# Optimization experiments

Measured on AMD Instinct MI355X. Metric: run time of the kernel, lower is better.

## Reference

```python
import jax, jax.numpy as jnp
import numpy as np

N_NODES = 100000


def setup_inputs() -> dict:
    key = jax.random.key(0)
    k1, k2, k3, k4, k5 = jax.random.split(key, 5)
    E = 3200000
    F_IN, F_OUT = 128, 128
    x = jax.random.normal(k1, (N_NODES, F_IN), dtype=jnp.float32)
    row = jax.random.randint(k2, (E,), 0, N_NODES, dtype=jnp.int32)
    col = jax.random.randint(k3, (E,), 0, N_NODES, dtype=jnp.int32)
    # normalized-adjacency-like positive values
    edge_vals = jax.random.uniform(k4, (E,), dtype=jnp.float32)
    # xavier_uniform for W, zeros for bias (reset_parameters)
    limit = float(np.sqrt(6.0 / (F_IN + F_OUT)))
    W = jax.random.uniform(k5, (F_IN, F_OUT), dtype=jnp.float32, minval=-limit, maxval=limit)
    b = jnp.zeros((F_OUT,), dtype=jnp.float32)
    return {"x": x, "row": row, "col": col, "edge_vals": edge_vals, "W": W, "b": b}


def reference(x, row, col, edge_vals, W, b):
    # SpMM: (A @ x) where A is COO (row, col, edge_vals) of shape [N, N]
    gathered = edge_vals[:, None] * x[col]            # [E, F_in] irregular gather
    ax = jax.ops.segment_sum(gathered, row, num_segments=N_NODES)  # [N, F_in]
    # dense GEMM + bias
    return ax @ W + b
```

## Files before the change

### kernel.cpp

```cpp
#include <hip/hip_runtime.h>


#define FDIM 128
#define RPB   64
#define NBMAX 2048
#define MAXB  2560
#define TILE  4096

typedef __attribute__((ext_vector_type(8))) short short8;
typedef __attribute__((ext_vector_type(4))) float f32x4;

__device__ __forceinline__ unsigned bf16rn(float f) {
    unsigned u = __float_as_uint(f);
    return (u + 0x7FFFu + ((u >> 16) & 1u)) >> 16;
}

__global__ __launch_bounds__(256) void prep_w(const float* __restrict__ W,
                                              ushort* __restrict__ wbf) {
    int i = blockIdx.x * 1024 + threadIdx.x;
#pragma unroll
    for (int t = 0; t < 4; ++t, i += 256) {
        int k = i >> 7, c = i & 127;
        wbf[(c * 256 + ((k * 2) ^ ((c & 7) << 4))) >> 1] = (ushort)bf16rn(W[i]);
    }
}

__global__ __launch_bounds__(256) void fat_gemm_binA(
        const float* __restrict__ x, const ushort* __restrict__ wbf,
        char* __restrict__ xwq, float* __restrict__ sglob,
        const int* __restrict__ row, const int* __restrict__ col,
        const float* __restrict__ ev,
        int* __restrict__ bucketcur, unsigned long long* __restrict__ bentry,
        int N, int E, int nb, int G1, int G2) {
    __shared__ char smem[32768];
    const int tid = threadIdx.x;
    const int bid = blockIdx.x;

    if (bid < G1) {
        {
            const uint4* wsrc = (const uint4*)wbf;
            uint4* wdst = (uint4*)smem;
#pragma unroll
            for (int i = 0; i < 8; ++i) wdst[i * 256 + tid] = wsrc[i * 256 + tid];
        }
        __syncthreads();

        const int w = tid >> 6, l = tid & 63;
        const int g = l >> 4, c = l & 15;
        const int rbase = bid * 64 + w * 16;
        const int arow = rbase + c;
        const int kgrp = g * 8;

        f32x4 acc[8];
#pragma unroll
        for (int nt = 0; nt < 8; ++nt) acc[nt] = (f32x4){0.f, 0.f, 0.f, 0.f};

#pragma unroll
        for (int kb = 0; kb < 4; ++kb) {
            short8 a;
            if (arow < N) {
                const float* xp = x + (size_t)arow * FDIM + kb * 32 + kgrp;
                float4 x0 = ((const float4*)xp)[0];
                float4 x1 = ((const float4*)xp)[1];
                a[0] = (short)bf16rn(x0.x); a[1] = (short)bf16rn(x0.y);
                a[2] = (short)bf16rn(x0.z); a[3] = (short)bf16rn(x0.w);
                a[4] = (short)bf16rn(x1.x); a[5] = (short)bf16rn(x1.y);
                a[6] = (short)bf16rn(x1.z); a[7] = (short)bf16rn(x1.w);
            } else {
#pragma unroll
                for (int j = 0; j < 8; ++j) a[j] = 0;
            }
            const int kbyte = kb * 64 + g * 16;
#pragma unroll
            for (int nt = 0; nt < 8; ++nt) {
                int cc = nt * 16 + c;
                short8 bfrag = *(const short8*)(smem + cc * 256 + (kbyte ^ ((cc & 7) << 4)));
                acc[nt] = __builtin_amdgcn_mfma_f32_16x16x32_bf16(a, bfrag, acc[nt], 0, 0, 0);
            }
        }

        __syncthreads();

        float sr[4], inv[4];
#pragma unroll
        for (int r = 0; r < 4; ++r) {
            float m = 0.f;
#pragma unroll
            for (int nt = 0; nt < 8; ++nt) m = fmaxf(m, fabsf(acc[nt][r]));
#pragma unroll
            for (int mk = 1; mk < 16; mk <<= 1) m = fmaxf(m, __shfl_xor(m, mk));
            sr[r]  = m * (1.0f / 127.0f);
            inv[r] = (m > 0.f) ? (127.0f / m) : 0.f;
        }
        if (c == 0) {
#pragma unroll
            for (int r = 0; r < 4; ++r) {
                int gr = rbase + g * 4 + r;
                if (gr < N) sglob[gr] = sr[r];
            }
        }
        char* qlds = smem + w * 2048;
#pragma unroll
        for (int r = 0; r < 4; ++r)
#pragma unroll
            for (int nt = 0; nt < 8; ++nt) {
                int qi = (int)rintf(acc[nt][r] * inv[r]);
                qlds[(g * 4 + r) * 128 + nt * 16 + c] = (char)qi;
            }
        __syncthreads();

        uint4* dst = (uint4*)(xwq + (size_t)bid * 8192);
        const uint4* srcq = (const uint4*)smem;
#pragma unroll
        for (int t = 0; t < 2; ++t) {
            int i = t * 256 + tid;
            if (bid * 64 + (i >> 3) < N) dst[i] = srcq[i];
        }
    } else {
        int* tcnt  = (int*)smem;
        int* tbase = (int*)(smem + NBMAX * 4);

        for (long long t0 = (long long)(bid - G1) * TILE; t0 < E;
             t0 += (long long)G2 * TILE) {
            for (int i = tid; i < nb; i += 256) tcnt[i] = 0;
            __syncthreads();

            unsigned long long pk[16];
            int rr[16];
#pragma unroll
            for (int j = 0; j < 16; ++j) {
                long long e = t0 + j * 256 + tid;
                if (e < E) {
                    int r = row[e];
                    int cc = col[e];
                    unsigned evu = __float_as_uint(ev[e]);
                    pk[j] = ((unsigned long long)(unsigned)r << 47) |
                            ((unsigned long long)(unsigned)cc << 30) |
                            (unsigned long long)(evu >> 2);
                    rr[j] = r;
                    atomicAdd(&tcnt[r >> 6], 1);
                } else {
                    rr[j] = -1;
                }
            }
            __syncthreads();

            for (int i = tid; i < nb; i += 256) {
                int cc = tcnt[i];
                tbase[i] = cc ? atomicAdd(&bucketcur[i], cc) : 0;
                tcnt[i] = 0;
            }
            __syncthreads();

#pragma unroll
            for (int j = 0; j < 16; ++j) {
                if (rr[j] >= 0) {
                    int bk = rr[j] >> 6;
                    int pos = tbase[bk] + atomicAdd(&tcnt[bk], 1);
                    if (pos < MAXB) bentry[(size_t)bk * MAXB + pos] = pk[j];
                }
            }
            __syncthreads();
        }
    }
}

#define PBATCH(B)                                                                \
    {                                                                            \
        int2 p[B];                                                               \
        _Pragma("unroll") for (int j = 0; j < B; ++j) p[j] = sent[e + 2*j + h];  \
        unsigned xv[B];                                                          \
        _Pragma("unroll") for (int j = 0; j < B; ++j)                            \
            xv[j] = *(const unsigned*)(xwq + (unsigned)p[j].x + loff);           \
        _Pragma("unroll") for (int j = 0; j < B; ++j) {                          \
            float v = __int_as_float(p[j].y);                                    \
            float fx = (float)(signed char)(xv[j] & 0xFF);                       \
            float fy = (float)(signed char)((xv[j] >> 8) & 0xFF);                \
            float fz = (float)(signed char)((xv[j] >> 16) & 0xFF);               \
            float fw = (float)(signed char)(xv[j] >> 24);                        \
            if (j & 1) {                                                         \
                a1.x = fmaf(v, fx, a1.x); a1.y = fmaf(v, fy, a1.y);              \
                a1.z = fmaf(v, fz, a1.z); a1.w = fmaf(v, fw, a1.w);              \
            } else {                                                             \
                a0.x = fmaf(v, fx, a0.x); a0.y = fmaf(v, fy, a0.y);              \
                a0.z = fmaf(v, fz, a0.z); a0.w = fmaf(v, fw, a0.w);              \
            }                                                                    \
        }                                                                        \
    }

__global__ __launch_bounds__(256) void sort_gather(
        const char* __restrict__ xwq, const float* __restrict__ sglob,
        const unsigned long long* __restrict__ bentry,
        const int* __restrict__ bucketcur,
        const float* __restrict__ bias, float* __restrict__ out, int N) {
    __shared__ int2 sent[MAXB];
    __shared__ int cnt[RPB];
    __shared__ int rs[RPB + 1];
    __shared__ int cur[RPB];
    const int tid = threadIdx.x;
    const int b = blockIdx.x;

    int sz = bucketcur[b];
    if (sz > MAXB) sz = MAXB;
    const unsigned long long* src = bentry + (size_t)b * MAXB;

    if (tid < RPB) cnt[tid] = 0;
    __syncthreads();

    unsigned long long pk[10];
    float sc[10];
#pragma unroll
    for (int k = 0; k < 10; ++k) {
        int i = tid + k * 256;
        if (i < sz) {
            unsigned long long p = src[i];
            pk[k] = p;
            atomicAdd(&cnt[(int)(p >> 47) & (RPB - 1)], 1);
            sc[k] = sglob[(unsigned)(p >> 30) & 0x1FFFFu];
        }
    }
    __syncthreads();

    if (tid < 64) {
        int v = cnt[tid];
        int s = v;
#pragma unroll
        for (int off = 1; off < 64; off <<= 1) {
            int t = __shfl_up(s, off);
            if (tid >= off) s += t;
        }
        rs[tid] = s - v;
        cur[tid] = s - v;
        if (tid == 63) rs[64] = s;
    }
    __syncthreads();

#pragma unroll
    for (int k = 0; k < 10; ++k) {
        int i = tid + k * 256;
        if (i < sz) {
            unsigned long long p = pk[k];
            int rib = (int)(p >> 47) & (RPB - 1);
            unsigned coff = (((unsigned)(p >> 30)) & 0x1FFFFu) << 7;
            float evf = __uint_as_float(((unsigned)p & 0x3FFFFFFFu) << 2);
            int pos = atomicAdd(&cur[rib], 1);
            sent[pos] = make_int2((int)coff, __float_as_int(evf * sc[k]));
        }
    }
    __syncthreads();

    const int lane = tid & 63;
    const int wid  = tid >> 6;
    const int h    = lane >> 5;
    const int s    = lane & 31;
    const unsigned loff = (unsigned)(s << 2);
    float4 bias4 = ((const float4*)bias)[s];
    const float4 zero4 = {0.f, 0.f, 0.f, 0.f};

    for (int rl = 0; rl < 16; ++rl) {
        const int rib = wid * 16 + rl;
        const int gr = b * RPB + rib;
        int e = rs[rib];
        const int end = rs[rib + 1];

        float4 a0 = (h == 0) ? bias4 : zero4;
        float4 a1 = zero4;

        for (; e + 8 <= end; e += 8) PBATCH(4)
        for (; e + 2 <= end; e += 2) PBATCH(1)
        if (e < end) {
            int2 p = sent[e];
            unsigned xv = *(const unsigned*)(xwq + (unsigned)p.x + loff);
            float v = (h == 0) ? __int_as_float(p.y) : 0.f;
            a0.x = fmaf(v, (float)(signed char)(xv & 0xFF), a0.x);
            a0.y = fmaf(v, (float)(signed char)((xv >> 8) & 0xFF), a0.y);
            a0.z = fmaf(v, (float)(signed char)((xv >> 16) & 0xFF), a0.z);
            a0.w = fmaf(v, (float)(signed char)(xv >> 24), a0.w);
        }

        float4 t;
        t.x = a0.x + a1.x; t.y = a0.y + a1.y;
        t.z = a0.z + a1.z; t.w = a0.w + a1.w;
        t.x += __shfl_xor(t.x, 32);
        t.y += __shfl_xor(t.y, 32);
        t.z += __shfl_xor(t.z, 32);
        t.w += __shfl_xor(t.w, 32);
        if (h == 0 && gr < N)
            *(float4*)(out + (size_t)gr * FDIM + s * 4) = t;
    }
}

extern "C" void kernel_launch(void* const* d_in, const int* in_sizes, int n_in,
                              void* d_out, int out_size, void* d_ws, size_t ws_size,
                              hipStream_t stream) {
    const float* x   = (const float*)d_in[0];
    const int*   row = (const int*)d_in[1];
    const int*   col = (const int*)d_in[2];
    const float* ev  = (const float*)d_in[3];
    const float* W   = (const float*)d_in[4];
    const float* b   = (const float*)d_in[5];

    const int N = in_sizes[0] / FDIM;
    const int E = in_sizes[1];
    const int nb = (N + RPB - 1) / RPB;
    const int G1 = (N + 63) / 64;
    const int G2 = (E + TILE - 1) / TILE;

    char* ws = (char*)d_ws;
    char*     xwq       = (char*)(ws);
    float*    sglob     = (float*)(ws + 12800000);
    int*      bucketcur = (int*)(ws + 13200128);
    unsigned long long* bentry = (unsigned long long*)(ws + 13208320);
    ushort*   wbf       = (ushort*)(ws + 45218560);
    float*    out       = (float*)d_out;

    hipMemsetAsync(bucketcur, 0, (size_t)nb * sizeof(int), stream);

    prep_w<<<16, 256, 0, stream>>>((const float*)d_in[4], wbf);
    fat_gemm_binA<<<G1 + G2, 256, 0, stream>>>(x, wbf, xwq, sglob, row, col, ev,
                                               bucketcur, bentry, N, E, nb, G1, G2);
    sort_gather<<<nb, 256, 0, stream>>>(xwq, sglob, bentry, bucketcur, b, out, N);
}
```

Before: 143.9 us.

## Split each 64-row bucket across two blocks in sort_gather

Launches two sort_gather blocks per 64-row bucket. Each block filters the bucket's entries by bit 52 (the upper/lower 32-row half), shrinking the shared sent array and doubling block count to raise occupancy and parallelism. Each block reads the full bucket but keeps only half, which doubles bucket reads. The gather loop is also unrolled deeper (batches of 16 with 8/4/2 tails). A SENTMAX clamp can silently drop edges if a half-bucket overflows.

```diff
diff --git a/kernel.cpp b/kernel.cpp
--- a/kernel.cpp
+++ b/kernel.cpp
@@ -2,9 +2,11 @@
 
 
 #define FDIM 128
-#define RPB   64
+#define BKR   64
+#define RPB   32
 #define NBMAX 2048
 #define MAXB  2560
+#define SENTMAX 1536
 #define TILE  4096
 
 typedef __attribute__((ext_vector_type(8))) short short8;
@@ -193,58 +195,67 @@
         const unsigned long long* __restrict__ bentry,
         const int* __restrict__ bucketcur,
         const float* __restrict__ bias, float* __restrict__ out, int N) {
-    __shared__ int2 sent[MAXB];
+    __shared__ int2 sent[SENTMAX];
     __shared__ int cnt[RPB];
     __shared__ int rs[RPB + 1];
     __shared__ int cur[RPB];
     const int tid = threadIdx.x;
     const int b = blockIdx.x;
-
-    int sz = bucketcur[b];
+    const int B = b >> 1;
+    const int H = b & 1;
+
+    int sz = bucketcur[B];
     if (sz > MAXB) sz = MAXB;
-    const unsigned long long* src = bentry + (size_t)b * MAXB;
+    const unsigned long long* src = bentry + (size_t)B * MAXB;
 
     if (tid < RPB) cnt[tid] = 0;
     __syncthreads();
 
     unsigned long long pk[10];
     float sc[10];
+    bool kp[10];
 #pragma unroll
     for (int k = 0; k < 10; ++k) {
+        kp[k] = false;
         int i = tid + k * 256;
         if (i < sz) {
             unsigned long long p = src[i];
-            pk[k] = p;
-            atomicAdd(&cnt[(int)(p >> 47) & (RPB - 1)], 1);
-            sc[k] = sglob[(unsigned)(p >> 30) & 0x1FFFFu];
+            if (((int)(p >> 52) & 1) == H) {
+                kp[k] = true;
+                pk[k] = p;
+                atomicAdd(&cnt[(int)(p >> 47) & (RPB - 1)], 1);
+                sc[k] = sglob[(unsigned)(p >> 30) & 0x1FFFFu];
+            }
         }
     }
     __syncthreads();
 
-    if (tid < 64) {
+    if (tid < 32) {
         int v = cnt[tid];
         int s = v;
 #pragma unroll
-        for (int off = 1; off < 64; off <<= 1) {
+        for (int off = 1; off < 32; off <<= 1) {
             int t = __shfl_up(s, off);
             if (tid >= off) s += t;
         }
-        rs[tid] = s - v;
-        cur[tid] = s - v;
-        if (tid == 63) rs[64] = s;
+        int excl = s - v;
+        if (excl > SENTMAX) excl = SENTMAX;
+        rs[tid] = excl;
+        cur[tid] = excl;
+        if (tid == 31) rs[RPB] = (s > SENTMAX) ? SENTMAX : s;
     }
     __syncthreads();
 
 #pragma unroll
     for (int k = 0; k < 10; ++k) {
-        int i = tid + k * 256;
-        if (i < sz) {
+        if (kp[k]) {
             unsigned long long p = pk[k];
             int rib = (int)(p >> 47) & (RPB - 1);
             unsigned coff = (((unsigned)(p >> 30)) & 0x1FFFFu) << 7;
             float evf = __uint_as_float(((unsigned)p & 0x3FFFFFFFu) << 2);
             int pos = atomicAdd(&cur[rib], 1);
-            sent[pos] = make_int2((int)coff, __float_as_int(evf * sc[k]));
+            if (pos < SENTMAX)
+                sent[pos] = make_int2((int)coff, __float_as_int(evf * sc[k]));
         }
     }
     __syncthreads();
@@ -257,17 +268,19 @@
     float4 bias4 = ((const float4*)bias)[s];
     const float4 zero4 = {0.f, 0.f, 0.f, 0.f};
 
-    for (int rl = 0; rl < 16; ++rl) {
-        const int rib = wid * 16 + rl;
+    for (int rl = 0; rl < 8; ++rl) {
+        const int rib = wid * 8 + rl;
         const int gr = b * RPB + rib;
         int e = rs[rib];
-        const int end = rs[rib + 1];
+        int end = rs[rib + 1];
 
         float4 a0 = (h == 0) ? bias4 : zero4;
         float4 a1 = zero4;
 
-        for (; e + 8 <= end; e += 8) PBATCH(4)
-        for (; e + 2 <= end; e += 2) PBATCH(1)
+        for (; e + 16 <= end; e += 16) PBATCH(8)
+        if (e + 8 <= end) { PBATCH(4) e += 8; }
+        if (e + 4 <= end) { PBATCH(2) e += 4; }
+        if (e + 2 <= end) { PBATCH(1) e += 2; }
         if (e < end) {
             int2 p = sent[e];
             unsigned xv = *(const unsigned*)(xwq + (unsigned)p.x + loff);
@@ -302,7 +315,7 @@
 
     const int N = in_sizes[0] / FDIM;
     const int E = in_sizes[1];
-    const int nb = (N + RPB - 1) / RPB;
+    const int nb = (N + BKR - 1) / BKR;
     const int G1 = (N + 63) / 64;
     const int G2 = (E + TILE - 1) / TILE;
 
@@ -319,5 +332,5 @@
     prep_w<<<16, 256, 0, stream>>>((const float*)d_in[4], wbf);
     fat_gemm_binA<<<G1 + G2, 256, 0, stream>>>(x, wbf, xwq, sglob, row, col, ev,
                                                bucketcur, bentry, N, E, nb, G1, G2);
-    sort_gather<<<nb, 256, 0, stream>>>(xwq, sglob, bentry, bucketcur, b, out, N);
-}
+    sort_gather<<<2 * nb, 256, 0, stream>>>(xwq, sglob, bentry, bucketcur, b, out, N);
+}
```

Result: faster. 140.3 us (median of 2 runs) (-2.5%).
